# Kernel tuning notes

Measured on AMD Instinct MI355X. Metric: run time of the kernel, lower is better.

Reference implementation:

```python
import jax, jax.numpy as jnp
import numpy as np

H = 8
DH = 64  # attention_head_size
HID = 512
NEG = -90000000000.0

def _lin(x, w, b):
    return x @ w + b

def _tfs(x):  # [N, HID] -> [H, N, DH]
    n = x.shape[0]
    return x.reshape(n, H, DH).transpose(1, 0, 2)

def _cross(q, ck, v, cv, mask, dw, db):
    # q: [H,N,DH], ck/cv: [H,M,DH], v: [H,N,DH], mask: [N,M]
    s = jnp.einsum('hnd,hmd->hnm', q, ck)
    s = s * mask[None, :, :] / jnp.sqrt(jnp.asarray(DH, s.dtype))
    s = jnp.where(s == 0.0, NEG, s)  # faithful zero->-inf hack
    p = jax.nn.softmax(s, axis=-1)
    ctx = v + jnp.einsum('hnm,hmd->hnd', p, cv)  # residual add of raw value
    n = ctx.shape[1]
    ctx = ctx.transpose(1, 0, 2).reshape(n, H * DH)
    return _lin(ctx, dw, db)

def setup_inputs() -> dict:
    key = jax.random.key(0)
    ks = jax.random.split(key, 24)
    N1, N2, D1 = 4096, 4096, 300
    d = {}
    d['h_head'] = jax.random.normal(ks[0], (N1, D1), jnp.float32)
    d['h_tail'] = jax.random.normal(ks[1], (N2, HID), jnp.float32)
    d['batch_head'] = jnp.sort(jax.random.randint(ks[2], (N1,), 0, 64))
    d['batch_tail'] = jnp.sort(jax.random.randint(ks[3], (N2,), 0, 64))
    def w(k, i, o):
        return jax.random.normal(k, (i, o), jnp.float32) / np.sqrt(i)
    d['map_w'] = w(ks[4], D1, HID); d['map_b'] = jnp.zeros((HID,), jnp.float32)
    names = ['q1', 'k1', 'v1', 'q2', 'k2', 'v2', 'd1', 'd2']
    for i, nm in enumerate(names):
        d[nm + '_w'] = w(ks[5 + i], HID, HID)
        d[nm + '_b'] = jnp.zeros((HID,), jnp.float32)
    return d

def reference(h_head, h_tail, batch_head, batch_tail,
              map_w, map_b,
              q1_w, q1_b, k1_w, k1_b, v1_w, v1_b,
              q2_w, q2_b, k2_w, k2_b, v2_w, v2_b,
              d1_w, d1_b, d2_w, d2_b):
    hh = _lin(h_head, map_w, map_b)  # n_dim1 != n_dim2 -> map
    q_h = _tfs(_lin(hh, q1_w, q1_b))
    k_h = _tfs(_lin(hh, k1_w, k1_b))
    v_h = _tfs(_lin(hh, v1_w, v1_b))
    q_t = _tfs(_lin(h_tail, q2_w, q2_b))
    k_t = _tfs(_lin(h_tail, k2_w, k2_b))
    v_t = _tfs(_lin(h_tail, v2_w, v2_b))
    mask = (batch_head[:, None] == batch_tail[None, :]).astype(jnp.float32)
    out_head = _cross(q_h, k_t, v_h, v_t, mask, d1_w, d1_b)
    out_tail = _cross(q_t, k_h, v_t, v_h, mask.T, d2_w, d2_b)
    return (out_head, out_tail)
```

## Files before the change

### kernel.cpp

```cpp
#include <hip/hip_runtime.h>
#include <hip/hip_bf16.h>
#include <math.h>


typedef __bf16 bf16x8 __attribute__((ext_vector_type(8)));
typedef float  f32x4  __attribute__((ext_vector_type(4)));

#define HID 512
#define NTOK 4096
#define KHEAD 384

#define AS1(p) ((const __attribute__((address_space(1))) void*)(p))
#define AS3(p) ((__attribute__((address_space(3))) void*)(p))

struct PrepArgs {
    const float *h_head, *h_tail;
    const int *bh, *bt;
    const float *map_w, *map_b;
    const float *q1_w, *q1_b, *k1_w, *k1_b, *v1_w, *v1_b;
    const float* tsrc[8];
    __bf16*      tdst[8];
    __bf16 *hh_bf, *ht_bf, *map_bf;
    float *fb, *zbuf;
    int* ranges;
};

__global__ __launch_bounds__(256) void prep_all(PrepArgs a) {
    const int q = blockIdx.x, z = blockIdx.z, tid = threadIdx.x;
    __shared__ __bf16 T[64][72];
    __shared__ float  sm[512];

    if (z == 0) {
        if (q >= 512) return;
        if (q == 0 && tid < 128) {
            int b = tid & 63;
            const int* arr = (tid < 64) ? a.bh : a.bt;
            int base = (tid < 64) ? 0 : 128;
            int lo = 0, hi = NTOK;
            while (lo < hi) { int mid = (lo + hi) >> 1; if (arr[mid] < b) lo = mid + 1; else hi = mid; }
            int start = lo;
            lo = 0; hi = NTOK;
            while (lo < hi) { int mid = (lo + hi) >> 1; if (arr[mid] <= b) lo = mid + 1; else hi = mid; }
            a.ranges[base + b] = start;
            a.ranges[base + 64 + b] = lo;
        }
        for (int idx = tid; idx < 8 * 48; idx += 256) {
            int r   = q * 8 + idx / 48;
            int col = (idx % 48) * 8;
            bf16x8 v;
            if (col + 8 <= 300) {
                float4 f0 = *(const float4*)&a.h_head[(size_t)r * 300 + col];
                float4 f1 = *(const float4*)&a.h_head[(size_t)r * 300 + col + 4];
                v[0]=(__bf16)f0.x; v[1]=(__bf16)f0.y; v[2]=(__bf16)f0.z; v[3]=(__bf16)f0.w;
                v[4]=(__bf16)f1.x; v[5]=(__bf16)f1.y; v[6]=(__bf16)f1.z; v[7]=(__bf16)f1.w;
            } else if (col < 300) {
                float4 f0 = *(const float4*)&a.h_head[(size_t)r * 300 + col];
                v[0]=(__bf16)f0.x; v[1]=(__bf16)f0.y; v[2]=(__bf16)f0.z; v[3]=(__bf16)f0.w;
                v[4]=(__bf16)0.f; v[5]=(__bf16)0.f; v[6]=(__bf16)0.f; v[7]=(__bf16)0.f;
            } else {
                #pragma unroll
                for (int j = 0; j < 8; ++j) v[j] = (__bf16)0.f;
            }
            *(bf16x8*)&a.hh_bf[(size_t)r * KHEAD + col] = v;
        }
    } else if (z == 1) {
        if (q >= 512) return;
        for (int idx = tid; idx < 8 * 64; idx += 256) {
            int r   = q * 8 + (idx >> 6);
            int col = (idx & 63) * 8;
            float4 f0 = *(const float4*)&a.h_tail[(size_t)r * 512 + col];
            float4 f1 = *(const float4*)&a.h_tail[(size_t)r * 512 + col + 4];
            bf16x8 v;
            v[0]=(__bf16)f0.x; v[1]=(__bf16)f0.y; v[2]=(__bf16)f0.z; v[3]=(__bf16)f0.w;
            v[4]=(__bf16)f1.x; v[5]=(__bf16)f1.y; v[6]=(__bf16)f1.z; v[7]=(__bf16)f1.w;
            *(bf16x8*)&a.ht_bf[(size_t)r * 512 + col] = v;
        }
    } else {
        if (q < 96) {
            int r = q * 4 + (tid >> 6);
            int col = (tid & 63) * 8;
            bf16x8 v;
            if (r < 300) {
                float4 f0 = *(const float4*)&a.map_w[(size_t)r * 512 + col];
                float4 f1 = *(const float4*)&a.map_w[(size_t)r * 512 + col + 4];
                v[0]=(__bf16)f0.x; v[1]=(__bf16)f0.y; v[2]=(__bf16)f0.z; v[3]=(__bf16)f0.w;
                v[4]=(__bf16)f1.x; v[5]=(__bf16)f1.y; v[6]=(__bf16)f1.z; v[7]=(__bf16)f1.w;
            } else {
                #pragma unroll
                for (int j = 0; j < 8; ++j) v[j] = (__bf16)0.f;
            }
            *(bf16x8*)&a.map_bf[(size_t)r * 512 + col] = v;
        } else if (q < 102) {
            sm[tid] = a.map_b[tid];
            sm[tid + 256] = a.map_b[tid + 256];
            __syncthreads();
            int m = q - 96;
            int x = m >> 1, half = m & 1;
            int n = half * 256 + tid;
            const float* xw = x == 0 ? a.q1_w : (x == 1 ? a.k1_w : a.v1_w);
            const float* xb = x == 0 ? a.q1_b : (x == 1 ? a.k1_b : a.v1_b);
            float s = xb[n];
            for (int j = 0; j < 512; ++j)
                s += sm[j] * xw[(size_t)j * 512 + n];
            a.fb[x * 512 + n] = s;
        } else if (q == 102) {
            a.zbuf[tid] = 0.f;
            a.zbuf[tid + 256] = 0.f;
        } else if (q < 103 + 512) {
            int t  = q - 103;
            int w  = t >> 6;
            int j2 = t & 63;
            int tn = (j2 & 7) * 64;
            int tk = (j2 >> 3) * 64;
            const float* src = a.tsrc[w];
            __bf16* dst = a.tdst[w];
            const int r0 = tid >> 4;
            const int c0 = (tid & 15) * 4;
            #pragma unroll
            for (int i = 0; i < 4; ++i) {
                int k = tk + r0 + i * 16;
                float4 v = *(const float4*)&src[(size_t)k * 512 + tn + c0];
                T[r0 + i * 16][c0 + 0] = (__bf16)v.x;
                T[r0 + i * 16][c0 + 1] = (__bf16)v.y;
                T[r0 + i * 16][c0 + 2] = (__bf16)v.z;
                T[r0 + i * 16][c0 + 3] = (__bf16)v.w;
            }
            __syncthreads();
            const int n  = tid >> 2;
            const int kk = (tid & 3) * 16;
            bf16x8 o0, o1;
            #pragma unroll
            for (int j = 0; j < 8; ++j) { o0[j] = T[kk + j][n]; o1[j] = T[kk + 8 + j][n]; }
            __bf16* dp = dst + (size_t)(tn + n) * 512 + tk + kk;
            *(bf16x8*)dp       = o0;
            *(bf16x8*)(dp + 8) = o1;
        }
    }
}

struct GemmJobs {
    const __bf16* A[6];
    const __bf16* W[6];
    const float*  bias[6];
    void*         C[6];
    int           Kp[6];
    int           ldC[6];
};

template <typename TC>
__global__ __launch_bounds__(256) void gemm128(GemmJobs jobs) {
    __shared__ __align__(16) __bf16 As[2][4096];
    __shared__ __align__(16) __bf16 Bs[2][4096];

    const int z = blockIdx.z;
    const __bf16* A    = jobs.A[z];
    const __bf16* W    = jobs.W[z];
    const float*  bias = jobs.bias[z];
    TC*           C    = (TC*)jobs.C[z];
    const int     Kp   = jobs.Kp[z];
    const int     ldC  = jobs.ldC[z];

    const int tid  = threadIdx.x;
    const int wave = tid >> 6;
    const int lane = tid & 63;
    const int quad = lane >> 4;
    const int l16  = lane & 15;
    const int wy   = wave >> 1;
    const int wx   = wave & 1;
    const int rowBase = blockIdx.y * 128;
    const int colBase = blockIdx.x * 128;

    const int s_row = tid >> 2;
    const int s_kc  = ((tid & 3) ^ ((s_row >> 1) & 3)) * 8;

    const __bf16* gA = A + (size_t)(rowBase + s_row) * Kp + s_kc;
    const __bf16* gB = W + (size_t)(colBase + s_row) * Kp + s_kc;
    const int waveOff = wave * 512;

    f32x4 acc[4][4] = {};
    const int nk = Kp >> 5;

    __builtin_amdgcn_global_load_lds(AS1(gA),                   AS3(&As[0][waveOff]),        16, 0, 0);
    __builtin_amdgcn_global_load_lds(AS1(gA + (size_t)64 * Kp), AS3(&As[0][2048 + waveOff]), 16, 0, 0);
    __builtin_amdgcn_global_load_lds(AS1(gB),                   AS3(&Bs[0][waveOff]),        16, 0, 0);
    __builtin_amdgcn_global_load_lds(AS1(gB + (size_t)64 * Kp), AS3(&Bs[0][2048 + waveOff]), 16, 0, 0);

    for (int i = 0; i < nk; ++i) {
        const int cur = i & 1;
        __syncthreads();

        if (i + 1 < nk) {
            const int kt = (i + 1) * 32;
            const int nx = cur ^ 1;
            __builtin_amdgcn_global_load_lds(AS1(gA + kt),                   AS3(&As[nx][waveOff]),        16, 0, 0);
            __builtin_amdgcn_global_load_lds(AS1(gA + kt + (size_t)64 * Kp), AS3(&As[nx][2048 + waveOff]), 16, 0, 0);
            __builtin_amdgcn_global_load_lds(AS1(gB + kt),                   AS3(&Bs[nx][waveOff]),        16, 0, 0);
            __builtin_amdgcn_global_load_lds(AS1(gB + kt + (size_t)64 * Kp), AS3(&Bs[nx][2048 + waveOff]), 16, 0, 0);
        }

        bf16x8 ar[4], br[4];
        #pragma unroll
        for (int ii = 0; ii < 4; ++ii) {
            const int ra = wy * 64 + ii * 16 + l16;
            ar[ii] = *(const bf16x8*)&As[cur][ra * 32 + ((quad ^ ((ra >> 1) & 3)) << 3)];
        }
        #pragma unroll
        for (int jj = 0; jj < 4; ++jj) {
            const int rb = wx * 64 + jj * 16 + l16;
            br[jj] = *(const bf16x8*)&Bs[cur][rb * 32 + ((quad ^ ((rb >> 1) & 3)) << 3)];
        }
        #pragma unroll
        for (int ii = 0; ii < 4; ++ii)
            #pragma unroll
            for (int jj = 0; jj < 4; ++jj)
                acc[ii][jj] = __builtin_amdgcn_mfma_f32_16x16x32_bf16(ar[ii], br[jj], acc[ii][jj], 0, 0, 0);
    }

    #pragma unroll
    for (int jj = 0; jj < 4; ++jj) {
        int col = colBase + wx * 64 + jj * 16 + l16;
        float bv = bias[col];
        #pragma unroll
        for (int ii = 0; ii < 4; ++ii) {
            #pragma unroll
            for (int r = 0; r < 4; ++r) {
                int row = rowBase + wy * 64 + ii * 16 + quad * 4 + r;
                C[(size_t)row * ldC + col] = (TC)(acc[ii][jj][r] + bv);
            }
        }
    }
}

__global__ __launch_bounds__(256) void attn_mfma(
    const __bf16* __restrict__ Q0, const __bf16* __restrict__ K0,
    const __bf16* __restrict__ Vr0, const __bf16* __restrict__ Vc0,
    const __bf16* __restrict__ Q1, const __bf16* __restrict__ K1,
    const __bf16* __restrict__ Vr1, const __bf16* __restrict__ Vc1,
    const int* __restrict__ ranges,
    __bf16* __restrict__ O0, __bf16* __restrict__ O1,
    int Nq, int Nk)
{
    __shared__ __align__(16) __bf16 Qs[64][72];
    __shared__ __align__(16) __bf16 Ks[128][72];
    __shared__ __align__(16) __bf16 Vt[64][136];
    __shared__ __align__(16) __bf16 Ps[64][136];

    const int z = blockIdx.z;
    const __bf16* Q    = z ? Q1 : Q0;
    const __bf16* Kg   = z ? K1 : K0;
    const __bf16* Vres = z ? Vr1 : Vr0;
    const __bf16* Vctx = z ? Vc1 : Vc0;
    __bf16* Out        = z ? O1 : O0;
    const int* qstart  = z ? ranges + 128 : ranges;
    const int* qend    = z ? ranges + 192 : ranges + 64;
    const int* kstart  = z ? ranges       : ranges + 128;
    const int* kend    = z ? ranges + 64  : ranges + 192;

    const int h = blockIdx.x, b = blockIdx.y;
    const int qs = qstart[b], qe = qend[b];
    const int ts = kstart[b], te = kend[b];
    const int nq = qe - qs, nk = te - ts;
    if (nq <= 0) return;

    const int tid  = threadIdx.x;
    const int wave = tid >> 6;
    const int lane = tid & 63;
    const int quad = lane >> 4;
    const int l16  = lane & 15;
    const int srow = tid >> 2;
    const int scol = (tid & 3) * 16;
    const int krow = tid >> 1;
    const int kcol = (tid & 1) * 32;

    if (nk <= 0) {
        float* meanv = (float*)Qs;
        if (tid < 64) {
            float s = 0.f;
            for (int m = 0; m < Nk; ++m)
                s += (float)Vctx[(size_t)m * HID + h * 64 + tid];
            meanv[tid] = s / (float)Nk;
        }
        __syncthreads();
        int d = tid & 63;
        for (int r = qs + (tid >> 6); r < qe; r += 4) {
            size_t off = (size_t)r * HID + h * 64 + d;
            Out[off] = (__bf16)((float)Vres[off] + meanv[d]);
        }
        return;
    }

    for (int qc = 0; qc < nq; qc += 64) {
        __syncthreads();
        {
            int qg = min(qs + qc + srow, Nq - 1);
            const __bf16* src = Q + (size_t)qg * HID + h * 64 + scol;
            *(bf16x8*)&Qs[srow][scol]     = *(const bf16x8*)src;
            *(bf16x8*)&Qs[srow][scol + 8] = *(const bf16x8*)(src + 8);
        }
        __syncthreads();
        bf16x8 aq0 = *(const bf16x8*)&Qs[wave * 16 + l16][quad * 8];
        bf16x8 aq1 = *(const bf16x8*)&Qs[wave * 16 + l16][32 + quad * 8];

        f32x4 O[4] = {};
        float Mx[4], L[4];
        #pragma unroll
        for (int r = 0; r < 4; ++r) { Mx[r] = -__builtin_inff(); L[r] = 0.f; }

        for (int kc = 0; kc < nk; kc += 128) {
            if (kc) __syncthreads();
            {
                int kg = min(ts + kc + krow, Nk - 1);
                const __bf16* ksrc = Kg + (size_t)kg * HID + h * 64 + kcol;
                bf16x8 k0 = *(const bf16x8*)ksrc;
                bf16x8 k1 = *(const bf16x8*)(ksrc + 8);
                bf16x8 k2 = *(const bf16x8*)(ksrc + 16);
                bf16x8 k3 = *(const bf16x8*)(ksrc + 24);
                *(bf16x8*)&Ks[krow][kcol]      = k0;
                *(bf16x8*)&Ks[krow][kcol + 8]  = k1;
                *(bf16x8*)&Ks[krow][kcol + 16] = k2;
                *(bf16x8*)&Ks[krow][kcol + 24] = k3;
                const __bf16* vsrc = Vctx + (size_t)kg * HID + h * 64 + kcol;
                bf16x8 v0 = *(const bf16x8*)vsrc;
                bf16x8 v1 = *(const bf16x8*)(vsrc + 8);
                bf16x8 v2 = *(const bf16x8*)(vsrc + 16);
                bf16x8 v3 = *(const bf16x8*)(vsrc + 24);
                #pragma unroll
                for (int j = 0; j < 8; ++j) {
                    Vt[kcol + j][krow]      = v0[j];
                    Vt[kcol + 8 + j][krow]  = v1[j];
                    Vt[kcol + 16 + j][krow] = v2[j];
                    Vt[kcol + 24 + j][krow] = v3[j];
                }
            }
            __syncthreads();

            f32x4 S[8];
            #pragma unroll
            for (int c = 0; c < 8; ++c) {
                S[c] = f32x4{0.f, 0.f, 0.f, 0.f};
                bf16x8 bk0 = *(const bf16x8*)&Ks[c * 16 + l16][quad * 8];
                bf16x8 bk1 = *(const bf16x8*)&Ks[c * 16 + l16][32 + quad * 8];
                S[c] = __builtin_amdgcn_mfma_f32_16x16x32_bf16(aq0, bk0, S[c], 0, 0, 0);
                S[c] = __builtin_amdgcn_mfma_f32_16x16x32_bf16(aq1, bk1, S[c], 0, 0, 0);
            }

            #pragma unroll
            for (int c = 0; c < 8; ++c) {
                bool valid = (ts + kc + c * 16 + l16) < te;
                #pragma unroll
                for (int r = 0; r < 4; ++r)
                    S[c][r] = valid ? S[c][r] * 0.125f : -__builtin_inff();
            }

            float cm[4], ps[4], alpha[4];
            #pragma unroll
            for (int r = 0; r < 4; ++r) {
                float v = S[0][r];
                #pragma unroll
                for (int c = 1; c < 8; ++c) v = fmaxf(v, S[c][r]);
                v = fmaxf(v, __shfl_xor(v, 1, 64));
                v = fmaxf(v, __shfl_xor(v, 2, 64));
                v = fmaxf(v, __shfl_xor(v, 4, 64));
                v = fmaxf(v, __shfl_xor(v, 8, 64));
                cm[r] = v;
            }
            #pragma unroll
            for (int r = 0; r < 4; ++r) {
                float nM = fmaxf(Mx[r], cm[r]);
                alpha[r] = __expf(Mx[r] - nM);
                Mx[r] = nM;
                ps[r] = 0.f;
            }
            #pragma unroll
            for (int c = 0; c < 8; ++c)
                #pragma unroll
                for (int r = 0; r < 4; ++r) {
                    float p = __expf(S[c][r] - Mx[r]);
                    S[c][r] = p;
                    ps[r] += p;
                }
            #pragma unroll
            for (int r = 0; r < 4; ++r) {
                float v = ps[r];
                v += __shfl_xor(v, 1, 64);
                v += __shfl_xor(v, 2, 64);
                v += __shfl_xor(v, 4, 64);
                v += __shfl_xor(v, 8, 64);
                L[r] = L[r] * alpha[r] + v;
            }
            #pragma unroll
            for (int c = 0; c < 4; ++c)
                #pragma unroll
                for (int r = 0; r < 4; ++r)
                    O[c][r] *= alpha[r];

            #pragma unroll
            for (int c = 0; c < 8; ++c)
                #pragma unroll
                for (int r = 0; r < 4; ++r)
                    Ps[wave * 16 + quad * 4 + r][c * 16 + l16] = (__bf16)S[c][r];
            __syncthreads();

            #pragma unroll
            for (int ks = 0; ks < 4; ++ks) {
                bf16x8 ap = *(const bf16x8*)&Ps[wave * 16 + l16][ks * 32 + quad * 8];
                #pragma unroll
                for (int cd = 0; cd < 4; ++cd) {
                    bf16x8 bv = *(const bf16x8*)&Vt[cd * 16 + l16][ks * 32 + quad * 8];
                    O[cd] = __builtin_amdgcn_mfma_f32_16x16x32_bf16(ap, bv, O[cd], 0, 0, 0);
                }
            }
        }

        #pragma unroll
        for (int c = 0; c < 4; ++c) {
            int d = h * 64 + c * 16 + l16;
            #pragma unroll
            for (int r = 0; r < 4; ++r) {
                int qrow = qs + qc + wave * 16 + quad * 4 + r;
                if (qrow < qe) {
                    size_t off = (size_t)qrow * HID + d;
                    Out[off] = (__bf16)((float)Vres[off] + O[c][r] / L[r]);
                }
            }
        }
    }
}

extern "C" void kernel_launch(void* const* d_in, const int* in_sizes, int n_in,
                              void* d_out, int out_size, void* d_ws, size_t ws_size,
                              hipStream_t stream) {
    (void)in_sizes; (void)n_in; (void)out_size; (void)ws_size;

    const float* h_head = (const float*)d_in[0];
    const float* h_tail = (const float*)d_in[1];
    const int* batch_head = (const int*)d_in[2];
    const int* batch_tail = (const int*)d_in[3];
    const float* map_w = (const float*)d_in[4];
    const float* map_b = (const float*)d_in[5];
    const float* q1_w = (const float*)d_in[6];
    const float* q1_b = (const float*)d_in[7];
    const float* k1_w = (const float*)d_in[8];
    const float* k1_b = (const float*)d_in[9];
    const float* v1_w = (const float*)d_in[10];
    const float* v1_b = (const float*)d_in[11];
    const float* q2_w = (const float*)d_in[12];
    const float* q2_b = (const float*)d_in[13];
    const float* k2_w = (const float*)d_in[14];
    const float* k2_b = (const float*)d_in[15];
    const float* v2_w = (const float*)d_in[16];
    const float* v2_b = (const float*)d_in[17];
    const float* d1_w = (const float*)d_in[18];
    const float* d1_b = (const float*)d_in[19];
    const float* d2_w = (const float*)d_in[20];
    const float* d2_b = (const float*)d_in[21];

    float* out = (float*)d_out;

    const size_t SZ = (size_t)NTOK * HID;
    char* ws = (char*)d_ws;
    int* ranges = (int*)ws;
    __bf16* qh   = (__bf16*)(ws + 1024);
    __bf16* kh   = qh  + SZ;
    __bf16* vh   = kh  + SZ;
    __bf16* qt   = vh  + SZ;
    __bf16* kt   = qt  + SZ;
    __bf16* vt   = kt  + SZ;
    __bf16* ctxh = vt  + SZ;
    __bf16* ctxt = ctxh + SZ;
    __bf16* q1T  = ctxt + SZ;
    __bf16* k1T  = q1T + 512 * 512;
    __bf16* v1T  = k1T + 512 * 512;
    __bf16* q2T  = v1T + 512 * 512;
    __bf16* k2T  = q2T + 512 * 512;
    __bf16* v2T  = k2T + 512 * 512;
    __bf16* d1T  = v2T + 512 * 512;
    __bf16* d2T  = d1T + 512 * 512;
    __bf16* hh_bf  = d2T + 512 * 512;
    __bf16* ht_bf  = hh_bf + (size_t)NTOK * KHEAD;
    __bf16* map_bf = ht_bf + SZ;
    __bf16* fwqT   = map_bf + 384 * 512;
    __bf16* fwkT   = fwqT + 512 * KHEAD;
    __bf16* fwvT   = fwkT + 512 * KHEAD;
    float*  fb     = (float*)(fwvT + 512 * KHEAD);
    float*  zbuf   = fb + 3 * 512;

    PrepArgs pa;
    pa.h_head = h_head; pa.h_tail = h_tail; pa.bh = batch_head; pa.bt = batch_tail;
    pa.map_w = map_w; pa.map_b = map_b;
    pa.q1_w = q1_w; pa.q1_b = q1_b; pa.k1_w = k1_w; pa.k1_b = k1_b;
    pa.v1_w = v1_w; pa.v1_b = v1_b;
    const float* wsrc[8] = {q1_w, k1_w, v1_w, q2_w, k2_w, v2_w, d1_w, d2_w};
    __bf16* wdst[8] = {q1T, k1T, v1T, q2T, k2T, v2T, d1T, d2T};
    for (int i = 0; i < 8; ++i) { pa.tsrc[i] = wsrc[i]; pa.tdst[i] = wdst[i]; }
    pa.hh_bf = hh_bf; pa.ht_bf = ht_bf; pa.map_bf = map_bf;
    pa.fb = fb; pa.zbuf = zbuf; pa.ranges = ranges;
    prep_all<<<dim3(615, 1, 3), dim3(256), 0, stream>>>(pa);

    {
        GemmJobs j = {};
        j.A[0] = q1T; j.W[0] = map_bf; j.bias[0] = zbuf; j.C[0] = fwqT; j.Kp[0] = 512; j.ldC[0] = KHEAD;
        j.A[1] = k1T; j.W[1] = map_bf; j.bias[1] = zbuf; j.C[1] = fwkT; j.Kp[1] = 512; j.ldC[1] = KHEAD;
        j.A[2] = v1T; j.W[2] = map_bf; j.bias[2] = zbuf; j.C[2] = fwvT; j.Kp[2] = 512; j.ldC[2] = KHEAD;
        gemm128<__bf16><<<dim3(3, 4, 3), dim3(256), 0, stream>>>(j);
    }

    {
        GemmJobs j = {};
        j.A[0] = hh_bf; j.W[0] = fwqT; j.bias[0] = fb;        j.C[0] = qh; j.Kp[0] = KHEAD; j.ldC[0] = 512;
        j.A[1] = hh_bf; j.W[1] = fwkT; j.bias[1] = fb + 512;  j.C[1] = kh; j.Kp[1] = KHEAD; j.ldC[1] = 512;
        j.A[2] = hh_bf; j.W[2] = fwvT; j.bias[2] = fb + 1024; j.C[2] = vh; j.Kp[2] = KHEAD; j.ldC[2] = 512;
        j.A[3] = ht_bf; j.W[3] = q2T;  j.bias[3] = q2_b;      j.C[3] = qt; j.Kp[3] = 512;   j.ldC[3] = 512;
        j.A[4] = ht_bf; j.W[4] = k2T;  j.bias[4] = k2_b;      j.C[4] = kt; j.Kp[4] = 512;   j.ldC[4] = 512;
        j.A[5] = ht_bf; j.W[5] = v2T;  j.bias[5] = v2_b;      j.C[5] = vt; j.Kp[5] = 512;   j.ldC[5] = 512;
        gemm128<__bf16><<<dim3(4, 32, 6), dim3(256), 0, stream>>>(j);
    }

    attn_mfma<<<dim3(8, 64, 2), dim3(256), 0, stream>>>(
        qh, kt, vh, vt,
        qt, kh, vt, vh,
        ranges, ctxh, ctxt, NTOK, NTOK);

    {
        GemmJobs j = {};
        j.A[0] = ctxh; j.W[0] = d1T; j.bias[0] = d1_b; j.C[0] = out;      j.Kp[0] = 512; j.ldC[0] = 512;
        j.A[1] = ctxt; j.W[1] = d2T; j.bias[1] = d2_b; j.C[1] = out + SZ; j.Kp[1] = 512; j.ldC[1] = 512;
        gemm128<float><<<dim3(4, 32, 2), dim3(256), 0, stream>>>(j);
    }
}
```

Measured before the change: 200.1 us.

## Unfuse map weight into head projections and switch to 64x128 GEMM tiles

```diff
diff --git a/kernel.cpp b/kernel.cpp
--- a/kernel.cpp
+++ b/kernel.cpp
@@ -8,7 +8,7 @@
 
 #define HID 512
 #define NTOK 4096
-#define KHEAD 384
+#define KHEAD 320
 
 #define AS1(p) ((const __attribute__((address_space(1))) void*)(p))
 #define AS3(p) ((__attribute__((address_space(3))) void*)(p))
@@ -16,19 +16,15 @@
 struct PrepArgs {
     const float *h_head, *h_tail;
     const int *bh, *bt;
-    const float *map_w, *map_b;
-    const float *q1_w, *q1_b, *k1_w, *k1_b, *v1_w, *v1_b;
-    const float* tsrc[8];
-    __bf16*      tdst[8];
-    __bf16 *hh_bf, *ht_bf, *map_bf;
-    float *fb, *zbuf;
+    const float* tsrc[9];
+    __bf16*      tdst[9];
+    __bf16 *hh_bf, *ht_bf;
     int* ranges;
 };
 
 __global__ __launch_bounds__(256) void prep_all(PrepArgs a) {
     const int q = blockIdx.x, z = blockIdx.z, tid = threadIdx.x;
     __shared__ __bf16 T[64][72];
-    __shared__ float  sm[512];
 
     if (z == 0) {
         if (q >= 512) return;
@@ -44,9 +40,9 @@
             a.ranges[base + b] = start;
             a.ranges[base + 64 + b] = lo;
         }
-        for (int idx = tid; idx < 8 * 48; idx += 256) {
-            int r   = q * 8 + idx / 48;
-            int col = (idx % 48) * 8;
+        for (int idx = tid; idx < 8 * 40; idx += 256) {
+            int r   = q * 8 + idx / 40;
+            int col = (idx % 40) * 8;
             bf16x8 v;
             if (col + 8 <= 300) {
                 float4 f0 = *(const float4*)&a.h_head[(size_t)r * 300 + col];
@@ -76,80 +72,50 @@
             *(bf16x8*)&a.ht_bf[(size_t)r * 512 + col] = v;
         }
     } else {
-        if (q < 96) {
-            int r = q * 4 + (tid >> 6);
-            int col = (tid & 63) * 8;
-            bf16x8 v;
-            if (r < 300) {
-                float4 f0 = *(const float4*)&a.map_w[(size_t)r * 512 + col];
-                float4 f1 = *(const float4*)&a.map_w[(size_t)r * 512 + col + 4];
-                v[0]=(__bf16)f0.x; v[1]=(__bf16)f0.y; v[2]=(__bf16)f0.z; v[3]=(__bf16)f0.w;
-                v[4]=(__bf16)f1.x; v[5]=(__bf16)f1.y; v[6]=(__bf16)f1.z; v[7]=(__bf16)f1.w;
-            } else {
-                #pragma unroll
-                for (int j = 0; j < 8; ++j) v[j] = (__bf16)0.f;
-            }
-            *(bf16x8*)&a.map_bf[(size_t)r * 512 + col] = v;
-        } else if (q < 102) {
-            sm[tid] = a.map_b[tid];
-            sm[tid + 256] = a.map_b[tid + 256];
-            __syncthreads();
-            int m = q - 96;
-            int x = m >> 1, half = m & 1;
-            int n = half * 256 + tid;
-            const float* xw = x == 0 ? a.q1_w : (x == 1 ? a.k1_w : a.v1_w);
-            const float* xb = x == 0 ? a.q1_b : (x == 1 ? a.k1_b : a.v1_b);
-            float s = xb[n];
-            for (int j = 0; j < 512; ++j)
-                s += sm[j] * xw[(size_t)j * 512 + n];
-            a.fb[x * 512 + n] = s;
-        } else if (q == 102) {
-            a.zbuf[tid] = 0.f;
-            a.zbuf[tid + 256] = 0.f;
-        } else if (q < 103 + 512) {
-            int t  = q - 103;
-            int w  = t >> 6;
-            int j2 = t & 63;
-            int tn = (j2 & 7) * 64;
-            int tk = (j2 >> 3) * 64;
-            const float* src = a.tsrc[w];
-            __bf16* dst = a.tdst[w];
-            const int r0 = tid >> 4;
-            const int c0 = (tid & 15) * 4;
-            #pragma unroll
-            for (int i = 0; i < 4; ++i) {
-                int k = tk + r0 + i * 16;
-                float4 v = *(const float4*)&src[(size_t)k * 512 + tn + c0];
-                T[r0 + i * 16][c0 + 0] = (__bf16)v.x;
-                T[r0 + i * 16][c0 + 1] = (__bf16)v.y;
-                T[r0 + i * 16][c0 + 2] = (__bf16)v.z;
-                T[r0 + i * 16][c0 + 3] = (__bf16)v.w;
-            }
-            __syncthreads();
-            const int n  = tid >> 2;
-            const int kk = (tid & 3) * 16;
-            bf16x8 o0, o1;
-            #pragma unroll
-            for (int j = 0; j < 8; ++j) { o0[j] = T[kk + j][n]; o1[j] = T[kk + 8 + j][n]; }
-            __bf16* dp = dst + (size_t)(tn + n) * 512 + tk + kk;
-            *(bf16x8*)dp       = o0;
-            *(bf16x8*)(dp + 8) = o1;
-        }
+        int w  = q >> 6;
+        int t  = q & 63;
+        int tn = (t & 7) * 64;
+        int tk = (t >> 3) * 64;
+        const int K   = (w == 0) ? 300 : 512;
+        const int ldT = (w == 0) ? KHEAD : 512;
+        if (tk >= ldT) return;
+        const float* src = a.tsrc[w];
+        __bf16* dst = a.tdst[w];
+        const int r0 = tid >> 4;
+        const int c0 = (tid & 15) * 4;
+        #pragma unroll
+        for (int i = 0; i < 4; ++i) {
+            int k = tk + r0 + i * 16;
+            float4 v = (k < K) ? *(const float4*)&src[(size_t)k * 512 + tn + c0]
+                               : float4{0.f, 0.f, 0.f, 0.f};
+            T[r0 + i * 16][c0 + 0] = (__bf16)v.x;
+            T[r0 + i * 16][c0 + 1] = (__bf16)v.y;
+            T[r0 + i * 16][c0 + 2] = (__bf16)v.z;
+            T[r0 + i * 16][c0 + 3] = (__bf16)v.w;
+        }
+        __syncthreads();
+        const int n  = tid >> 2;
+        const int kk = (tid & 3) * 16;
+        bf16x8 o0, o1;
+        #pragma unroll
+        for (int j = 0; j < 8; ++j) { o0[j] = T[kk + j][n]; o1[j] = T[kk + 8 + j][n]; }
+        __bf16* dp = dst + (size_t)(tn + n) * ldT + tk + kk;
+        *(bf16x8*)dp       = o0;
+        *(bf16x8*)(dp + 8) = o1;
     }
 }
 
 struct GemmJobs {
-    const __bf16* A[6];
-    const __bf16* W[6];
-    const float*  bias[6];
-    void*         C[6];
-    int           Kp[6];
-    int           ldC[6];
+    const __bf16* A[4];
+    const __bf16* W[4];
+    const float*  bias[4];
+    void*         C[4];
+    int           Kp[4];
 };
 
 template <typename TC>
-__global__ __launch_bounds__(256) void gemm128(GemmJobs jobs) {
-    __shared__ __align__(16) __bf16 As[2][4096];
+__global__ __launch_bounds__(256) void gemm64x128(GemmJobs jobs) {
+    __shared__ __align__(16) __bf16 As[2][2048];
     __shared__ __align__(16) __bf16 Bs[2][4096];
 
     const int z = blockIdx.z;
@@ -158,7 +124,6 @@
     const float*  bias = jobs.bias[z];
     TC*           C    = (TC*)jobs.C[z];
     const int     Kp   = jobs.Kp[z];
-    const int     ldC  = jobs.ldC[z];
 
     const int tid  = threadIdx.x;
     const int wave = tid >> 6;
@@ -167,7 +132,7 @@
     const int l16  = lane & 15;
     const int wy   = wave >> 1;
     const int wx   = wave & 1;
-    const int rowBase = blockIdx.y * 128;
+    const int rowBase = blockIdx.y * 64;
     const int colBase = blockIdx.x * 128;
 
     const int s_row = tid >> 2;
@@ -177,11 +142,10 @@
     const __bf16* gB = W + (size_t)(colBase + s_row) * Kp + s_kc;
     const int waveOff = wave * 512;
 
-    f32x4 acc[4][4] = {};
+    f32x4 acc[2][4] = {};
     const int nk = Kp >> 5;
 
     __builtin_amdgcn_global_load_lds(AS1(gA),                   AS3(&As[0][waveOff]),        16, 0, 0);
-    __builtin_amdgcn_global_load_lds(AS1(gA + (size_t)64 * Kp), AS3(&As[0][2048 + waveOff]), 16, 0, 0);
     __builtin_amdgcn_global_load_lds(AS1(gB),                   AS3(&Bs[0][waveOff]),        16, 0, 0);
     __builtin_amdgcn_global_load_lds(AS1(gB + (size_t)64 * Kp), AS3(&Bs[0][2048 + waveOff]), 16, 0, 0);
 
@@ -193,15 +157,14 @@
             const int kt = (i + 1) * 32;
             const int nx = cur ^ 1;
             __builtin_amdgcn_global_load_lds(AS1(gA + kt),                   AS3(&As[nx][waveOff]),        16, 0, 0);
-            __builtin_amdgcn_global_load_lds(AS1(gA + kt + (size_t)64 * Kp), AS3(&As[nx][2048 + waveOff]), 16, 0, 0);
             __builtin_amdgcn_global_load_lds(AS1(gB + kt),                   AS3(&Bs[nx][waveOff]),        16, 0, 0);
             __builtin_amdgcn_global_load_lds(AS1(gB + kt + (size_t)64 * Kp), AS3(&Bs[nx][2048 + waveOff]), 16, 0, 0);
         }
 
-        bf16x8 ar[4], br[4];
-        #pragma unroll
-        for (int ii = 0; ii < 4; ++ii) {
-            const int ra = wy * 64 + ii * 16 + l16;
+        bf16x8 ar[2], br[4];
+        #pragma unroll
+        for (int ii = 0; ii < 2; ++ii) {
+            const int ra = wy * 32 + ii * 16 + l16;
             ar[ii] = *(const bf16x8*)&As[cur][ra * 32 + ((quad ^ ((ra >> 1) & 3)) << 3)];
         }
         #pragma unroll
@@ -210,7 +173,7 @@
             br[jj] = *(const bf16x8*)&Bs[cur][rb * 32 + ((quad ^ ((rb >> 1) & 3)) << 3)];
         }
         #pragma unroll
-        for (int ii = 0; ii < 4; ++ii)
+        for (int ii = 0; ii < 2; ++ii)
             #pragma unroll
             for (int jj = 0; jj < 4; ++jj)
                 acc[ii][jj] = __builtin_amdgcn_mfma_f32_16x16x32_bf16(ar[ii], br[jj], acc[ii][jj], 0, 0, 0);
@@ -221,11 +184,11 @@
         int col = colBase + wx * 64 + jj * 16 + l16;
         float bv = bias[col];
         #pragma unroll
-        for (int ii = 0; ii < 4; ++ii) {
+        for (int ii = 0; ii < 2; ++ii) {
             #pragma unroll
             for (int r = 0; r < 4; ++r) {
-                int row = rowBase + wy * 64 + ii * 16 + quad * 4 + r;
-                C[(size_t)row * ldC + col] = (TC)(acc[ii][jj][r] + bv);
+                int row = rowBase + wy * 32 + ii * 16 + quad * 4 + r;
+                C[(size_t)row * HID + col] = (TC)(acc[ii][jj][r] + bv);
             }
         }
     }
@@ -460,7 +423,8 @@
     const size_t SZ = (size_t)NTOK * HID;
     char* ws = (char*)d_ws;
     int* ranges = (int*)ws;
-    __bf16* qh   = (__bf16*)(ws + 1024);
+    __bf16* hh   = (__bf16*)(ws + 1024);
+    __bf16* qh   = hh  + SZ;
     __bf16* kh   = qh  + SZ;
     __bf16* vh   = kh  + SZ;
     __bf16* qt   = vh  + SZ;
@@ -468,7 +432,8 @@
     __bf16* vt   = kt  + SZ;
     __bf16* ctxh = vt  + SZ;
     __bf16* ctxt = ctxh + SZ;
-    __bf16* q1T  = ctxt + SZ;
+    __bf16* mapT = ctxt + SZ;
+    __bf16* q1T  = mapT + 512 * KHEAD;
     __bf16* k1T  = q1T + 512 * 512;
     __bf16* v1T  = k1T + 512 * 512;
     __bf16* q2T  = v1T + 512 * 512;
@@ -476,44 +441,33 @@
     __bf16* v2T  = k2T + 512 * 512;
     __bf16* d1T  = v2T + 512 * 512;
     __bf16* d2T  = d1T + 512 * 512;
-    __bf16* hh_bf  = d2T + 512 * 512;
-    __bf16* ht_bf  = hh_bf + (size_t)NTOK * KHEAD;
-    __bf16* map_bf = ht_bf + SZ;
-    __bf16* fwqT   = map_bf + 384 * 512;
-    __bf16* fwkT   = fwqT + 512 * KHEAD;
-    __bf16* fwvT   = fwkT + 512 * KHEAD;
-    float*  fb     = (float*)(fwvT + 512 * KHEAD);
-    float*  zbuf   = fb + 3 * 512;
+    __bf16* hh_bf = d2T + 512 * 512;
+    __bf16* ht_bf = hh_bf + (size_t)NTOK * KHEAD;
 
     PrepArgs pa;
     pa.h_head = h_head; pa.h_tail = h_tail; pa.bh = batch_head; pa.bt = batch_tail;
-    pa.map_w = map_w; pa.map_b = map_b;
-    pa.q1_w = q1_w; pa.q1_b = q1_b; pa.k1_w = k1_w; pa.k1_b = k1_b;
-    pa.v1_w = v1_w; pa.v1_b = v1_b;
+    pa.tsrc[0] = map_w; pa.tdst[0] = mapT;
     const float* wsrc[8] = {q1_w, k1_w, v1_w, q2_w, k2_w, v2_w, d1_w, d2_w};
     __bf16* wdst[8] = {q1T, k1T, v1T, q2T, k2T, v2T, d1T, d2T};
-    for (int i = 0; i < 8; ++i) { pa.tsrc[i] = wsrc[i]; pa.tdst[i] = wdst[i]; }
-    pa.hh_bf = hh_bf; pa.ht_bf = ht_bf; pa.map_bf = map_bf;
-    pa.fb = fb; pa.zbuf = zbuf; pa.ranges = ranges;
-    prep_all<<<dim3(615, 1, 3), dim3(256), 0, stream>>>(pa);
+    for (int i = 0; i < 8; ++i) { pa.tsrc[i + 1] = wsrc[i]; pa.tdst[i + 1] = wdst[i]; }
+    pa.hh_bf = hh_bf; pa.ht_bf = ht_bf; pa.ranges = ranges;
+    prep_all<<<dim3(576, 1, 3), dim3(256), 0, stream>>>(pa);
 
     {
-        GemmJobs j = {};
-        j.A[0] = q1T; j.W[0] = map_bf; j.bias[0] = zbuf; j.C[0] = fwqT; j.Kp[0] = 512; j.ldC[0] = KHEAD;
-        j.A[1] = k1T; j.W[1] = map_bf; j.bias[1] = zbuf; j.C[1] = fwkT; j.Kp[1] = 512; j.ldC[1] = KHEAD;
-        j.A[2] = v1T; j.W[2] = map_bf; j.bias[2] = zbuf; j.C[2] = fwvT; j.Kp[2] = 512; j.ldC[2] = KHEAD;
-        gemm128<__bf16><<<dim3(3, 4, 3), dim3(256), 0, stream>>>(j);
-    }
-
+        GemmJobs j;
+        j.A[0] = hh_bf; j.W[0] = mapT; j.bias[0] = map_b; j.C[0] = hh; j.Kp[0] = KHEAD;
+        j.A[1] = ht_bf; j.W[1] = q2T;  j.bias[1] = q2_b;  j.C[1] = qt; j.Kp[1] = 512;
+        j.A[2] = ht_bf; j.W[2] = k2T;  j.bias[2] = k2_b;  j.C[2] = kt; j.Kp[2] = 512;
+        j.A[3] = ht_bf; j.W[3] = v2T;  j.bias[3] = v2_b;  j.C[3] = vt; j.Kp[3] = 512;
+        gemm64x128<__bf16><<<dim3(4, 64, 4), dim3(256), 0, stream>>>(j);
+    }
     {
-        GemmJobs j = {};
-        j.A[0] = hh_bf; j.W[0] = fwqT; j.bias[0] = fb;        j.C[0] = qh; j.Kp[0] = KHEAD; j.ldC[0] = 512;
-        j.A[1] = hh_bf; j.W[1] = fwkT; j.bias[1] = fb + 512;  j.C[1] = kh; j.Kp[1] = KHEAD; j.ldC[1] = 512;
-        j.A[2] = hh_bf; j.W[2] = fwvT; j.bias[2] = fb + 1024; j.C[2] = vh; j.Kp[2] = KHEAD; j.ldC[2] = 512;
-        j.A[3] = ht_bf; j.W[3] = q2T;  j.bias[3] = q2_b;      j.C[3] = qt; j.Kp[3] = 512;   j.ldC[3] = 512;
-        j.A[4] = ht_bf; j.W[4] = k2T;  j.bias[4] = k2_b;      j.C[4] = kt; j.Kp[4] = 512;   j.ldC[4] = 512;
-        j.A[5] = ht_bf; j.W[5] = v2T;  j.bias[5] = v2_b;      j.C[5] = vt; j.Kp[5] = 512;   j.ldC[5] = 512;
-        gemm128<__bf16><<<dim3(4, 32, 6), dim3(256), 0, stream>>>(j);
+        GemmJobs j;
+        j.A[0] = hh; j.W[0] = q1T; j.bias[0] = q1_b; j.C[0] = qh; j.Kp[0] = 512;
+        j.A[1] = hh; j.W[1] = k1T; j.bias[1] = k1_b; j.C[1] = kh; j.Kp[1] = 512;
+        j.A[2] = hh; j.W[2] = v1T; j.bias[2] = v1_b; j.C[2] = vh; j.Kp[2] = 512;
+        j.A[3] = hh; j.W[3] = v1T; j.bias[3] = v1_b; j.C[3] = vh; j.Kp[3] = 512;
+        gemm64x128<__bf16><<<dim3(4, 64, 3), dim3(256), 0, stream>>>(j);
     }
 
     attn_mfma<<<dim3(8, 64, 2), dim3(256), 0, stream>>>(
@@ -522,9 +476,11 @@
         ranges, ctxh, ctxt, NTOK, NTOK);
 
     {
-        GemmJobs j = {};
-        j.A[0] = ctxh; j.W[0] = d1T; j.bias[0] = d1_b; j.C[0] = out;      j.Kp[0] = 512; j.ldC[0] = 512;
-        j.A[1] = ctxt; j.W[1] = d2T; j.bias[1] = d2_b; j.C[1] = out + SZ; j.Kp[1] = 512; j.ldC[1] = 512;
-        gemm128<float><<<dim3(4, 32, 2), dim3(256), 0, stream>>>(j);
+        GemmJobs j;
+        j.A[0] = ctxh; j.W[0] = d1T; j.bias[0] = d1_b; j.C[0] = out;      j.Kp[0] = 512;
+        j.A[1] = ctxt; j.W[1] = d2T; j.bias[1] = d2_b; j.C[1] = out + SZ; j.Kp[1] = 512;
+        j.A[2] = ctxt; j.W[2] = d2T; j.bias[2] = d2_b; j.C[2] = out + SZ; j.Kp[2] = 512;
+        j.A[3] = ctxt; j.W[3] = d2T; j.bias[3] = d2_b; j.C[3] = out + SZ; j.Kp[3] = 512;
+        gemm64x128<float><<<dim3(4, 64, 2), dim3(256), 0, stream>>>(j);
     }
 }
```

New measurement: 187.2 us. -6.4%, faster.
